# Kernel optimization log

Measured on AMD Instinct MI355X. Metric: run time of the kernel, lower is better.

The kernel has to match this reference:

```python
import jax, jax.numpy as jnp
import numpy as np

N = 100000       # nodes
E0 = 1600000     # random edges (self-loops appended -> E = E0 + N)
IN = 128         # input feature dim
H1, C1 = 8, 8    # conv1 heads, out channels per head
C2 = 64          # num_classes (conv2 out, heads=1)
NEG_SLOPE = 0.2


def gat_conv(x, src, dst, W, att_src, att_dst, bias, heads, out_ch, concat):
    """PyG-style GATConv (eval mode, no dropout). x: [N, F_in]."""
    n = x.shape[0]
    h = (x @ W).reshape(n, heads, out_ch)              # [N, H, C]
    a_src = jnp.sum(h * att_src, axis=-1)              # [N, H]
    a_dst = jnp.sum(h * att_dst, axis=-1)              # [N, H]
    e = jax.nn.leaky_relu(a_src[src] + a_dst[dst], NEG_SLOPE)  # [E, H]
    # segment softmax over edges grouped by destination node
    e_max = jax.ops.segment_max(e, dst, num_segments=n)
    ex = jnp.exp(e - e_max[dst])
    denom = jax.ops.segment_sum(ex, dst, num_segments=n)
    alpha = ex / denom[dst]                            # [E, H]
    msg = h[src] * alpha[:, :, None]                   # [E, H, C]
    out = jax.ops.segment_sum(msg, dst, num_segments=n)  # [N, H, C]
    out = out.reshape(n, heads * out_ch) if concat else out.mean(axis=1)
    return out + bias


def setup_inputs() -> dict:
    key = jax.random.key(0)
    ks = jax.random.split(key, 12)
    nodes = jnp.arange(N, dtype=jnp.int32)
    feat = jax.random.normal(ks[0], (N, IN), jnp.float32)
    src = jax.random.randint(ks[1], (E0,), 0, N, jnp.int32)
    dst = jax.random.randint(ks[2], (E0,), 0, N, jnp.int32)
    loop = jnp.arange(N, dtype=jnp.int32)
    edge_index = jnp.stack([jnp.concatenate([src, loop]),
                            jnp.concatenate([dst, loop])])  # [2, E]
    mask = jnp.ones((N,), bool)
    label = jax.random.randint(ks[3], (N,), 0, C2, jnp.int32)
    s = 0.1
    W1 = jax.random.normal(ks[4], (IN, H1 * C1), jnp.float32) * s
    att_src1 = jax.random.normal(ks[5], (H1, C1), jnp.float32) * s
    att_dst1 = jax.random.normal(ks[6], (H1, C1), jnp.float32) * s
    b1 = jnp.zeros((H1 * C1,), jnp.float32)
    W2 = jax.random.normal(ks[7], (H1 * C1, C2), jnp.float32) * s
    att_src2 = jax.random.normal(ks[8], (1, C2), jnp.float32) * s
    att_dst2 = jax.random.normal(ks[9], (1, C2), jnp.float32) * s
    b2 = jnp.zeros((C2,), jnp.float32)
    return {"nodes": nodes, "feat": feat, "edge_index": edge_index, "mask": mask,
            "label": label, "W1": W1, "att_src1": att_src1, "att_dst1": att_dst1,
            "b1": b1, "W2": W2, "att_src2": att_src2, "att_dst2": att_dst2, "b2": b2}


def reference(nodes, feat, edge_index, mask, label,
              W1, att_src1, att_dst1, b1, W2, att_src2, att_dst2, b2):
    src, dst = edge_index[0], edge_index[1]
    x = jax.nn.elu(gat_conv(feat, src, dst, W1, att_src1, att_dst1, b1,
                            H1, C1, concat=True))          # [N, 64]
    scores = gat_conv(x, src, dst, W2, att_src2, att_dst2, b2,
                      1, C2, concat=False)                  # [N, C2]
    logp = jax.nn.log_softmax(scores, axis=-1)
    nll = -jnp.take_along_axis(logp, label[:, None].astype(jnp.int32), axis=1)[:, 0]
    m = mask.astype(scores.dtype)
    loss = jnp.sum(nll * m) / jnp.sum(m)                    # masked mean CE
    pred = jnp.argmax(scores, axis=1)
    return loss, pred, label
```

## Files before the change

### kernel.cpp

```cpp
#include <hip/hip_runtime.h>
#include <cstdint>

#define NHEAD 8
#define D1 64
#define IN_F 128
#define NEG 0.2f
#define NBINS 256
#define BINS 1024
#define BSH 7
#define CHUNK 8192

__device__ __forceinline__ void fma4(float4& a, float s, const float4& v)
{
    a.x = fmaf(s, v.x, a.x); a.y = fmaf(s, v.y, a.y);
    a.z = fmaf(s, v.z, a.z); a.w = fmaf(s, v.w, a.w);
}

__global__ __launch_bounds__(256) void k_gemm1_hist(
    const float* __restrict__ feat,
    const float* __restrict__ W1,
    const float* __restrict__ att_s,
    const float* __restrict__ att_d,
    float* __restrict__ h1, float* __restrict__ a_src, float* __restrict__ a_dst,
    const int* __restrict__ dst, int* __restrict__ btot, int* __restrict__ bh,
    int N, int E, int GH)
{
    __shared__ float Wh[32 * 64];
    __shared__ float Fh[64 * 36];
    const int tid = threadIdx.x;

    if ((int)blockIdx.x < GH) {
        int* hist = (int*)Wh;
        for (int b = tid; b < BINS; b += 256) hist[b] = 0;
        __syncthreads();
        const int e0 = blockIdx.x * CHUNK;
        #pragma unroll
        for (int r = 0; r < 8; ++r) {
            int e = e0 + r * 1024 + tid * 4;
            if (e + 3 < E) {
                int4 d4 = *(const int4*)&dst[e];
                atomicAdd(&hist[d4.x >> BSH], 1);
                atomicAdd(&hist[d4.y >> BSH], 1);
                atomicAdd(&hist[d4.z >> BSH], 1);
                atomicAdd(&hist[d4.w >> BSH], 1);
            } else {
                for (int k = e; k < E && k < e + 4; ++k)
                    atomicAdd(&hist[dst[k] >> BSH], 1);
            }
        }
        __syncthreads();
        for (int b = tid; b < BINS; b += 256) {
            int c = hist[b];
            bh[(size_t)blockIdx.x * BINS + b] = c;
            if (c) atomicAdd(&btot[b * 16], c);
        }
        return;
    }

    const int tx = tid & 15, ty = tid >> 4;
    const int base = (blockIdx.x - GH) * 64;
    float4 acc0 = {0,0,0,0}, acc1 = {0,0,0,0}, acc2 = {0,0,0,0}, acc3 = {0,0,0,0};

    for (int p = 0; p < 4; ++p) {
        if (p) __syncthreads();
        for (int i = tid; i < 32 * 64; i += 256)
            Wh[i] = W1[p * 2048 + i];
        for (int i = tid; i < 64 * 32; i += 256) {
            int r = i >> 5, kk = i & 31;
            int n = base + r;
            Fh[r * 36 + kk] = (n < N) ? feat[(size_t)n * IN_F + p * 32 + kk] : 0.f;
        }
        __syncthreads();
        const float* wk = &Wh[4 * tx];
        const float* f0 = &Fh[(4 * ty + 0) * 36];
        const float* f1 = &Fh[(4 * ty + 1) * 36];
        const float* f2 = &Fh[(4 * ty + 2) * 36];
        const float* f3 = &Fh[(4 * ty + 3) * 36];
        #pragma unroll
        for (int kk = 0; kk < 32; kk += 4) {
            float4 fa = *(const float4*)&f0[kk];
            float4 fb = *(const float4*)&f1[kk];
            float4 fc = *(const float4*)&f2[kk];
            float4 fd = *(const float4*)&f3[kk];
            float4 w0 = *(const float4*)&wk[(kk + 0) * 64];
            float4 w1 = *(const float4*)&wk[(kk + 1) * 64];
            float4 w2 = *(const float4*)&wk[(kk + 2) * 64];
            float4 w3 = *(const float4*)&wk[(kk + 3) * 64];
            fma4(acc0, fa.x, w0); fma4(acc0, fa.y, w1); fma4(acc0, fa.z, w2); fma4(acc0, fa.w, w3);
            fma4(acc1, fb.x, w0); fma4(acc1, fb.y, w1); fma4(acc1, fb.z, w2); fma4(acc1, fb.w, w3);
            fma4(acc2, fc.x, w0); fma4(acc2, fc.y, w1); fma4(acc2, fc.z, w2); fma4(acc2, fc.w, w3);
            fma4(acc3, fd.x, w0); fma4(acc3, fd.y, w1); fma4(acc3, fd.z, w2); fma4(acc3, fd.w, w3);
        }
    }
    const float4 as4 = *(const float4*)&att_s[4 * tx];
    const float4 ad4 = *(const float4*)&att_d[4 * tx];
    float4 accs[4] = {acc0, acc1, acc2, acc3};
    #pragma unroll
    for (int i = 0; i < 4; ++i) {
        int n = base + 4 * ty + i;
        if (n < N) {
            *(float4*)&h1[(size_t)n * D1 + 4 * tx] = accs[i];
            float ps = accs[i].x * as4.x + accs[i].y * as4.y + accs[i].z * as4.z + accs[i].w * as4.w;
            float pd = accs[i].x * ad4.x + accs[i].y * ad4.y + accs[i].z * ad4.z + accs[i].w * ad4.w;
            ps += __shfl_xor(ps, 1);
            pd += __shfl_xor(pd, 1);
            if ((tx & 1) == 0) {
                a_src[n * NHEAD + (tx >> 1)] = ps;
                a_dst[n * NHEAD + (tx >> 1)] = pd;
            }
        }
    }
}

__device__ __forceinline__ int block_incl_scan(int v, int tid, int* lds4)
{
    int lane = tid & 63, w = tid >> 6;
    #pragma unroll
    for (int off = 1; off < 64; off <<= 1) {
        int t = __shfl_up(v, off);
        if (lane >= off) v += t;
    }
    if (lane == 63) lds4[w] = v;
    __syncthreads();
    int add = 0;
    #pragma unroll
    for (int i = 0; i < 4; ++i)
        if (i < w) add += lds4[i];
    __syncthreads();
    return v + add;
}

__global__ __launch_bounds__(256) void k_bscan(
    const int* __restrict__ btot, int* __restrict__ bbase, int* __restrict__ gcur,
    double* __restrict__ bins)
{
    __shared__ int lds4[4];
    const int tid = threadIdx.x;
    bins[tid] = 0.0;
    int c0 = btot[(4 * tid + 0) * 16];
    int c1 = btot[(4 * tid + 1) * 16];
    int c2 = btot[(4 * tid + 2) * 16];
    int c3 = btot[(4 * tid + 3) * 16];
    int v = c0 + c1 + c2 + c3;
    int incl = block_incl_scan(v, tid, lds4);
    int b0 = incl - v, b1 = b0 + c0, b2 = b1 + c1, b3 = b2 + c2;
    bbase[4 * tid + 0] = b0; gcur[(4 * tid + 0) * 16] = b0;
    bbase[4 * tid + 1] = b1; gcur[(4 * tid + 1) * 16] = b1;
    bbase[4 * tid + 2] = b2; gcur[(4 * tid + 2) * 16] = b2;
    bbase[4 * tid + 3] = b3; gcur[(4 * tid + 3) * 16] = b3;
}

__global__ __launch_bounds__(256) void k_scatter(
    const int* __restrict__ src, const int* __restrict__ dst,
    const int* __restrict__ bh, int* __restrict__ gcur,
    int* __restrict__ bucketed, int E)
{
    __shared__ int base[BINS], cur[BINS];
    const int tid = threadIdx.x;
    for (int b = tid; b < BINS; b += 256) {
        cur[b] = 0;
        int c = bh[(size_t)blockIdx.x * BINS + b];
        if (c) base[b] = atomicAdd(&gcur[b * 16], c);
    }
    __syncthreads();
    const int e0 = blockIdx.x * CHUNK;
    #pragma unroll
    for (int r = 0; r < 8; ++r) {
        int e = e0 + r * 1024 + tid * 4;
        if (e + 3 < E) {
            int4 d4 = *(const int4*)&dst[e];
            int4 s4 = *(const int4*)&src[e];
            int bx, rx;
            bx = d4.x >> BSH; rx = atomicAdd(&cur[bx], 1); bucketed[base[bx] + rx] = ((d4.x & 127) << 17) | s4.x;
            bx = d4.y >> BSH; rx = atomicAdd(&cur[bx], 1); bucketed[base[bx] + rx] = ((d4.y & 127) << 17) | s4.y;
            bx = d4.z >> BSH; rx = atomicAdd(&cur[bx], 1); bucketed[base[bx] + rx] = ((d4.z & 127) << 17) | s4.z;
            bx = d4.w >> BSH; rx = atomicAdd(&cur[bx], 1); bucketed[base[bx] + rx] = ((d4.w & 127) << 17) | s4.w;
        } else {
            for (int k = e; k < E && k < e + 4; ++k) {
                int d = dst[k];
                int bx = d >> BSH;
                int rx = atomicAdd(&cur[bx], 1);
                bucketed[base[bx] + rx] = ((d & 127) << 17) | src[k];
            }
        }
    }
}

__global__ __launch_bounds__(256) void k_seg(
    const int* __restrict__ btot, const int* __restrict__ bbase,
    const int* __restrict__ bucketed,
    int* __restrict__ deg, int* __restrict__ rowstart, int* __restrict__ srcs, int N)
{
    __shared__ int cnt[128], cur[128], lb[128];
    const int tid = threadIdx.x;
    const int b = blockIdx.x;
    const int gs = bbase[b];
    const int sz = btot[b * 16];
    if (tid < 128) { cnt[tid] = 0; cur[tid] = 0; }
    __syncthreads();
    for (int i = tid; i < sz; i += 256)
        atomicAdd(&cnt[bucketed[gs + i] >> 17], 1);
    __syncthreads();
    if (tid < 128) lb[tid] = cnt[tid];
    __syncthreads();
    #pragma unroll
    for (int off = 1; off < 128; off <<= 1) {
        int t = 0;
        if (tid < 128 && tid >= off) t = lb[tid - off];
        __syncthreads();
        if (tid < 128 && tid >= off) lb[tid] += t;
        __syncthreads();
    }
    if (tid < 128) {
        int ex = lb[tid] - cnt[tid];
        lb[tid] = ex;
        int d = b * 128 + tid;
        if (d < N) { deg[d] = cnt[tid]; rowstart[d] = gs + ex; }
    }
    __syncthreads();
    for (int i = tid; i < sz; i += 256) {
        int v = bucketed[gs + i];
        int d7 = v >> 17;
        int r = atomicAdd(&cur[d7], 1);
        srcs[gs + lb[d7] + r] = v & 0x1FFFF;
    }
}

__global__ __launch_bounds__(256) void k_agg1(
    const int* __restrict__ deg, const int* __restrict__ rowstart,
    const int* __restrict__ srcs,
    const float* __restrict__ a_s, const float* __restrict__ a_d,
    const float* __restrict__ h1, const float* __restrict__ b1,
    float* __restrict__ x, int N)
{
    const int tid = threadIdx.x, w = tid >> 6, j = tid & 63;
    const int c = j & 7, hh = j >> 3;
    const int t = j & 15, q = j >> 4;
    const int n = blockIdx.x * 4 + w;
    if (n >= N) return;
    const int rlen = deg[n];
    const int row = rowstart[n];
    const float ad = a_d[n * NHEAD + hh];
    float4 acc = {0.f, 0.f, 0.f, 0.f};
    float den = 0.f;
    int m = rlen < 8 ? rlen : 8;
    int myS   = (c < m) ? srcs[row + c] : 0;
    float av  = (c < m) ? a_s[myS * NHEAD + hh] : 0.f;
    for (int base = 0; base < rlen; base += 8) {
        int mn = rlen - base - 8; if (mn > 8) mn = 8; if (mn < 0) mn = 0;
        int   myS_n = (c < mn) ? srcs[row + base + 8 + c] : 0;
        float av_n  = (c < mn) ? a_s[myS_n * NHEAD + hh] : 0.f;
        float ex = 0.f;
        if (c < m) {
            float v = av + ad;
            v = v > 0.f ? v : NEG * v;
            ex = expf(v);
        }
        float ds = ex;
        ds += __shfl_xor(ds, 1);
        ds += __shfl_xor(ds, 2);
        ds += __shfl_xor(ds, 4);
        den += ds;
        int   s0 = __shfl(myS, 2 * q);
        int   s1 = __shfl(myS, 2 * q + 1);
        float e0 = __shfl(ex, ((t >> 1) << 3) | (2 * q));
        float e1 = __shfl(ex, ((t >> 1) << 3) | (2 * q + 1));
        float4 l0 = *(const float4*)&h1[(size_t)s0 * D1 + 4 * t];
        float4 l1 = *(const float4*)&h1[(size_t)s1 * D1 + 4 * t];
        fma4(acc, e0, l0);
        fma4(acc, e1, l1);
        myS = myS_n; av = av_n; m = mn;
    }
    acc.x += __shfl_xor(acc.x, 16); acc.y += __shfl_xor(acc.y, 16);
    acc.z += __shfl_xor(acc.z, 16); acc.w += __shfl_xor(acc.w, 16);
    acc.x += __shfl_xor(acc.x, 32); acc.y += __shfl_xor(acc.y, 32);
    acc.z += __shfl_xor(acc.z, 32); acc.w += __shfl_xor(acc.w, 32);
    float dd = __shfl(den, (t >> 1) << 3);
    if (q == 0) {
        float4 b = *(const float4*)&b1[4 * t];
        float4 o;
        o.x = acc.x / dd + b.x; o.y = acc.y / dd + b.y;
        o.z = acc.z / dd + b.z; o.w = acc.w / dd + b.w;
        o.x = o.x > 0.f ? o.x : expm1f(o.x);
        o.y = o.y > 0.f ? o.y : expm1f(o.y);
        o.z = o.z > 0.f ? o.z : expm1f(o.z);
        o.w = o.w > 0.f ? o.w : expm1f(o.w);
        *(float4*)&x[(size_t)n * D1 + 4 * t] = o;
    }
}

__global__ __launch_bounds__(256) void k_gemm2(
    const float* __restrict__ x,
    const float* __restrict__ W2,
    const float* __restrict__ att_s,
    const float* __restrict__ att_d,
    float* __restrict__ h2, float* __restrict__ a_src, float* __restrict__ a_dst,
    int N)
{
    __shared__ float Wh[64 * 64];
    __shared__ float Fh[64 * 68];
    const int tid = threadIdx.x;
    const int tx = tid & 15, ty = tid >> 4;
    const int base = blockIdx.x * 64;
    for (int i = tid; i < 64 * 64; i += 256)
        Wh[i] = W2[i];
    for (int i = tid; i < 64 * 64; i += 256) {
        int r = i >> 6, kk = i & 63;
        int n = base + r;
        Fh[r * 68 + kk] = (n < N) ? x[(size_t)n * 64 + kk] : 0.f;
    }
    __syncthreads();
    float4 acc0 = {0,0,0,0}, acc1 = {0,0,0,0}, acc2 = {0,0,0,0}, acc3 = {0,0,0,0};
    const float* wk = &Wh[4 * tx];
    const float* f0 = &Fh[(4 * ty + 0) * 68];
    const float* f1 = &Fh[(4 * ty + 1) * 68];
    const float* f2 = &Fh[(4 * ty + 2) * 68];
    const float* f3 = &Fh[(4 * ty + 3) * 68];
    #pragma unroll 4
    for (int kk = 0; kk < 64; kk += 4) {
        float4 fa = *(const float4*)&f0[kk];
        float4 fb = *(const float4*)&f1[kk];
        float4 fc = *(const float4*)&f2[kk];
        float4 fd = *(const float4*)&f3[kk];
        float4 w0 = *(const float4*)&wk[(kk + 0) * 64];
        float4 w1 = *(const float4*)&wk[(kk + 1) * 64];
        float4 w2 = *(const float4*)&wk[(kk + 2) * 64];
        float4 w3 = *(const float4*)&wk[(kk + 3) * 64];
        fma4(acc0, fa.x, w0); fma4(acc0, fa.y, w1); fma4(acc0, fa.z, w2); fma4(acc0, fa.w, w3);
        fma4(acc1, fb.x, w0); fma4(acc1, fb.y, w1); fma4(acc1, fb.z, w2); fma4(acc1, fb.w, w3);
        fma4(acc2, fc.x, w0); fma4(acc2, fc.y, w1); fma4(acc2, fc.z, w2); fma4(acc2, fc.w, w3);
        fma4(acc3, fd.x, w0); fma4(acc3, fd.y, w1); fma4(acc3, fd.z, w2); fma4(acc3, fd.w, w3);
    }
    const float4 as4 = *(const float4*)&att_s[4 * tx];
    const float4 ad4 = *(const float4*)&att_d[4 * tx];
    float4 accs[4] = {acc0, acc1, acc2, acc3};
    #pragma unroll
    for (int i = 0; i < 4; ++i) {
        int n = base + 4 * ty + i;
        if (n < N) {
            *(float4*)&h2[(size_t)n * 64 + 4 * tx] = accs[i];
            float ps = accs[i].x * as4.x + accs[i].y * as4.y + accs[i].z * as4.z + accs[i].w * as4.w;
            float pd = accs[i].x * ad4.x + accs[i].y * ad4.y + accs[i].z * ad4.z + accs[i].w * ad4.w;
            ps += __shfl_xor(ps, 1); pd += __shfl_xor(pd, 1);
            ps += __shfl_xor(ps, 2); pd += __shfl_xor(pd, 2);
            ps += __shfl_xor(ps, 4); pd += __shfl_xor(pd, 4);
            ps += __shfl_xor(ps, 8); pd += __shfl_xor(pd, 8);
            if (tx == 0) { a_src[n] = ps; a_dst[n] = pd; }
        }
    }
}

__global__ __launch_bounds__(256) void k_agg2(
    const int* __restrict__ deg, const int* __restrict__ rowstart,
    const int* __restrict__ srcs,
    const float* __restrict__ a_s, const float* __restrict__ a_d,
    const float* __restrict__ h2, const float* __restrict__ b2,
    const int* __restrict__ label,
    float* __restrict__ dout, double* __restrict__ bins, int N)
{
    __shared__ int2 sx[4][64];
    __shared__ float snll[16];
    const int tid = threadIdx.x, w = tid >> 6, j = tid & 63;
    const int t = j & 15, g16 = j & 0x30;
    const int n = blockIdx.x * 16 + (tid >> 4);
    if (tid < 16) snll[tid] = 0.f;
    __syncthreads();
    const bool valid = (n < N);
    const int rlen = valid ? deg[n] : 0;
    const int row  = valid ? rowstart[n] : 0;
    const float ad = valid ? a_d[n] : 0.f;
    float4 acc = {0.f, 0.f, 0.f, 0.f};
    float den = 0.f;
    for (int base = 0; base < rlen; base += 16) {
        int m = rlen - base; if (m > 16) m = 16;
        int myS = 0; float ex = 0.f;
        if (t < m) {
            myS = srcs[row + base + t];
            float v = a_s[myS] + ad;
            v = v > 0.f ? v : NEG * v;
            ex = expf(v);
        }
        float ds = ex;
        ds += __shfl_xor(ds, 1); ds += __shfl_xor(ds, 2);
        ds += __shfl_xor(ds, 4); ds += __shfl_xor(ds, 8);
        den += ds;
        sx[w][j] = make_int2(myS, __float_as_int(ex));
        asm volatile("s_waitcnt lgkmcnt(0)" ::: "memory");
        for (int kb = 0; kb < m; kb += 4) {
            int2 p0 = sx[w][g16 | (kb + 0)];
            int2 p1 = sx[w][g16 | (kb + 1)];
            int2 p2 = sx[w][g16 | (kb + 2)];
            int2 p3 = sx[w][g16 | (kb + 3)];
            float4 l0 = *(const float4*)&h2[(size_t)p0.x * 64 + 4 * t];
            float4 l1 = *(const float4*)&h2[(size_t)p1.x * 64 + 4 * t];
            float4 l2 = *(const float4*)&h2[(size_t)p2.x * 64 + 4 * t];
            float4 l3 = *(const float4*)&h2[(size_t)p3.x * 64 + 4 * t];
            fma4(acc, __int_as_float(p0.y), l0);
            fma4(acc, __int_as_float(p1.y), l1);
            fma4(acc, __int_as_float(p2.y), l2);
            fma4(acc, __int_as_float(p3.y), l3);
        }
        asm volatile("s_waitcnt lgkmcnt(0)" ::: "memory");
    }
    float4 b = *(const float4*)&b2[4 * t];
    float4 sc;
    sc.x = acc.x / den + b.x; sc.y = acc.y / den + b.y;
    sc.z = acc.z / den + b.z; sc.w = acc.w / den + b.w;
    float mv = sc.x; int mi = 4 * t;
    if (sc.y > mv) { mv = sc.y; mi = 4 * t + 1; }
    if (sc.z > mv) { mv = sc.z; mi = 4 * t + 2; }
    if (sc.w > mv) { mv = sc.w; mi = 4 * t + 3; }
    #pragma unroll
    for (int off = 1; off < 16; off <<= 1) {
        float ov = __shfl_xor(mv, off);
        int oi = __shfl_xor(mi, off);
        if (ov > mv || (ov == mv && oi < mi)) { mv = ov; mi = oi; }
    }
    float se = expf(sc.x - mv) + expf(sc.y - mv) + expf(sc.z - mv) + expf(sc.w - mv);
    #pragma unroll
    for (int off = 1; off < 16; off <<= 1) se += __shfl_xor(se, off);
    int lab = valid ? label[n] : 0;
    int comp = lab & 3;
    float cl = comp == 0 ? sc.x : comp == 1 ? sc.y : comp == 2 ? sc.z : sc.w;
    float sl = __shfl(cl, g16 | (lab >> 2));
    if (t == 0 && valid) {
        snll[tid >> 4] = mv + logf(se) - sl;
        dout[1 + n] = (float)mi;
        dout[1 + (size_t)N + n] = (float)lab;
    }
    __syncthreads();
    if (tid == 0) {
        double bs = 0.0;
        #pragma unroll
        for (int i = 0; i < 16; ++i) bs += (double)snll[i];
        atomicAdd(&bins[blockIdx.x & (NBINS - 1)], bs);
    }
}

__global__ __launch_bounds__(256) void k_loss(
    const double* __restrict__ bins, float* __restrict__ dout, int N)
{
    __shared__ double sw[4];
    const int tid = threadIdx.x;
    double v = bins[tid];
    #pragma unroll
    for (int off = 1; off < 64; off <<= 1) v += __shfl_xor(v, off);
    if ((tid & 63) == 0) sw[tid >> 6] = v;
    __syncthreads();
    if (tid == 0)
        dout[0] = (float)((sw[0] + sw[1] + sw[2] + sw[3]) / (double)N);
}

extern "C" void kernel_launch(void* const* d_in, const int* in_sizes, int n_in,
                              void* d_out, int out_size, void* d_ws, size_t ws_size,
                              hipStream_t stream)
{
    const float* feat   = (const float*)d_in[1];
    const int*   edge   = (const int*)d_in[2];
    const int*   label  = (const int*)d_in[4];
    const float* W1     = (const float*)d_in[5];
    const float* att_s1 = (const float*)d_in[6];
    const float* att_d1 = (const float*)d_in[7];
    const float* b1     = (const float*)d_in[8];
    const float* W2     = (const float*)d_in[9];
    const float* att_s2 = (const float*)d_in[10];
    const float* att_d2 = (const float*)d_in[11];
    const float* b2     = (const float*)d_in[12];

    const int N = in_sizes[0];
    const int E = in_sizes[2] / 2;
    const int* src = edge;
    const int* dst = edge + E;

    float* bufA = (float*)d_ws;
    float* bufB = bufA + (size_t)N * 64;
    float* a_s1 = bufB + (size_t)N * 64;
    float* a_d1 = a_s1 + (size_t)N * 8;
    int*   deg  = (int*)(a_d1 + (size_t)N * 8);
    int*   rowstart = deg + N;
    int*   srcs = rowstart + N;
    double* bins = (double*)(((uintptr_t)(srcs + E) + 7) & ~(uintptr_t)7);

    int* bucketed = (int*)bufB;
    int* btot  = bucketed + E;
    int* gcur  = btot + BINS * 16;
    int* bbase = gcur + BINS * 16;
    int* bh    = bbase + BINS;

    float* a_s2 = a_s1;
    float* a_d2 = a_s1 + N;

    float* out = (float*)d_out;

    const int GH    = (E + CHUNK - 1) / CHUNK;
    const int G1    = (N + 63) / 64;
    const int NBUCK = (N + 127) / 128;

    hipMemsetAsync(btot, 0, (size_t)BINS * 16 * sizeof(int), stream);

    k_gemm1_hist<<<GH + G1, 256, 0, stream>>>(feat, W1, att_s1, att_d1,
                                              bufA, a_s1, a_d1,
                                              dst, btot, bh, N, E, GH);
    k_bscan  <<<1, 256, 0, stream>>>(btot, bbase, gcur, bins);
    k_scatter<<<GH, 256, 0, stream>>>(src, dst, bh, gcur, bucketed, E);
    k_seg    <<<NBUCK, 256, 0, stream>>>(btot, bbase, bucketed, deg, rowstart, srcs, N);

    k_agg1 <<<(N + 3) / 4, 256, 0, stream>>>(deg, rowstart, srcs, a_s1, a_d1,
                                             bufA, b1, bufB, N);
    k_gemm2<<<G1, 256, 0, stream>>>(bufB, W2, att_s2, att_d2, bufA, a_s2, a_d2, N);
    k_agg2 <<<(N + 15) / 16, 256, 0, stream>>>(deg, rowstart, srcs, a_s2, a_d2,
                                               bufA, b2, label, out, bins, N);
    k_loss <<<1, 256, 0, stream>>>(bins, out, N);
}
```

Baseline: 397.8 us.

## Process 16 edges per wave in layer-1 aggregation with LDS-shared attention weights

Restructures the layer-1 aggregation kernel so that each wave handles 16 edges per iteration instead of 8. Each lane computes two heads' exp weights and stages them in shared memory, then each quarter-wave gathers four source rows per iteration. The per-head denominator is now accumulated alongside the features and reduced with shuffles, which removes the cross-lane shuffle reductions per edge batch. Fast __expf also replaces expf in both aggregation kernels, trading some accuracy for cheaper exponentials.

Result: no change. 390.3 us (-1.9%).

```diff
diff --git a/kernel.cpp b/kernel.cpp
--- a/kernel.cpp
+++ b/kernel.cpp
@@ -233,54 +233,60 @@
     const float* __restrict__ h1, const float* __restrict__ b1,
     float* __restrict__ x, int N)
 {
+    __shared__ float sex[4][128];
     const int tid = threadIdx.x, w = tid >> 6, j = tid & 63;
-    const int c = j & 7, hh = j >> 3;
     const int t = j & 15, q = j >> 4;
     const int n = blockIdx.x * 4 + w;
     if (n >= N) return;
     const int rlen = deg[n];
     const int row = rowstart[n];
-    const float ad = a_d[n * NHEAD + hh];
+    const float2 ad2 = *(const float2*)&a_d[n * NHEAD + 2 * q];
+    const int h = t >> 1;
+    float* sw = sex[w];
     float4 acc = {0.f, 0.f, 0.f, 0.f};
     float den = 0.f;
-    int m = rlen < 8 ? rlen : 8;
-    int myS   = (c < m) ? srcs[row + c] : 0;
-    float av  = (c < m) ? a_s[myS * NHEAD + hh] : 0.f;
-    for (int base = 0; base < rlen; base += 8) {
-        int mn = rlen - base - 8; if (mn > 8) mn = 8; if (mn < 0) mn = 0;
-        int   myS_n = (c < mn) ? srcs[row + base + 8 + c] : 0;
-        float av_n  = (c < mn) ? a_s[myS_n * NHEAD + hh] : 0.f;
-        float ex = 0.f;
-        if (c < m) {
-            float v = av + ad;
-            v = v > 0.f ? v : NEG * v;
-            ex = expf(v);
-        }
-        float ds = ex;
-        ds += __shfl_xor(ds, 1);
-        ds += __shfl_xor(ds, 2);
-        ds += __shfl_xor(ds, 4);
-        den += ds;
-        int   s0 = __shfl(myS, 2 * q);
-        int   s1 = __shfl(myS, 2 * q + 1);
-        float e0 = __shfl(ex, ((t >> 1) << 3) | (2 * q));
-        float e1 = __shfl(ex, ((t >> 1) << 3) | (2 * q + 1));
-        float4 l0 = *(const float4*)&h1[(size_t)s0 * D1 + 4 * t];
-        float4 l1 = *(const float4*)&h1[(size_t)s1 * D1 + 4 * t];
-        fma4(acc, e0, l0);
-        fma4(acc, e1, l1);
-        myS = myS_n; av = av_n; m = mn;
+    bool v = (t < rlen);
+    int   s  = v ? srcs[row + t] : 0;
+    float2 a2 = v ? *(const float2*)&a_s[s * NHEAD + 2 * q] : make_float2(0.f, 0.f);
+    for (int base = 0; base < rlen; base += 16) {
+        bool vn = (base + 16 + t < rlen);
+        int   sn  = vn ? srcs[row + base + 16 + t] : 0;
+        float2 an = vn ? *(const float2*)&a_s[sn * NHEAD + 2 * q] : make_float2(0.f, 0.f);
+        float e0 = 0.f, e1 = 0.f;
+        if (v) {
+            float x0 = a2.x + ad2.x; x0 = x0 > 0.f ? x0 : NEG * x0; e0 = __expf(x0);
+            float x1 = a2.y + ad2.y; x1 = x1 > 0.f ? x1 : NEG * x1; e1 = __expf(x1);
+        }
+        *(float2*)&sw[t * 8 + 2 * q] = make_float2(e0, e1);
+        asm volatile("s_waitcnt lgkmcnt(0)" ::: "memory");
+        int mTot = rlen - base;
+        if (4 * q < mTot) {
+            int s0 = __shfl(s, 4 * q + 0), s1 = __shfl(s, 4 * q + 1);
+            int s2 = __shfl(s, 4 * q + 2), s3 = __shfl(s, 4 * q + 3);
+            float w0 = sw[(4 * q + 0) * 8 + h], w1 = sw[(4 * q + 1) * 8 + h];
+            float w2 = sw[(4 * q + 2) * 8 + h], w3 = sw[(4 * q + 3) * 8 + h];
+            float4 l0 = *(const float4*)&h1[(size_t)s0 * D1 + 4 * t];
+            float4 l1 = *(const float4*)&h1[(size_t)s1 * D1 + 4 * t];
+            float4 l2 = *(const float4*)&h1[(size_t)s2 * D1 + 4 * t];
+            float4 l3 = *(const float4*)&h1[(size_t)s3 * D1 + 4 * t];
+            fma4(acc, w0, l0); fma4(acc, w1, l1);
+            fma4(acc, w2, l2); fma4(acc, w3, l3);
+            den += (w0 + w1) + (w2 + w3);
+        }
+        asm volatile("s_waitcnt lgkmcnt(0)" ::: "memory");
+        v = vn; s = sn; a2 = an;
     }
     acc.x += __shfl_xor(acc.x, 16); acc.y += __shfl_xor(acc.y, 16);
     acc.z += __shfl_xor(acc.z, 16); acc.w += __shfl_xor(acc.w, 16);
+    den   += __shfl_xor(den, 16);
     acc.x += __shfl_xor(acc.x, 32); acc.y += __shfl_xor(acc.y, 32);
     acc.z += __shfl_xor(acc.z, 32); acc.w += __shfl_xor(acc.w, 32);
-    float dd = __shfl(den, (t >> 1) << 3);
+    den   += __shfl_xor(den, 32);
     if (q == 0) {
         float4 b = *(const float4*)&b1[4 * t];
         float4 o;
-        o.x = acc.x / dd + b.x; o.y = acc.y / dd + b.y;
-        o.z = acc.z / dd + b.z; o.w = acc.w / dd + b.w;
+        o.x = acc.x / den + b.x; o.y = acc.y / den + b.y;
+        o.z = acc.z / den + b.z; o.w = acc.w / den + b.w;
         o.x = o.x > 0.f ? o.x : expm1f(o.x);
         o.y = o.y > 0.f ? o.y : expm1f(o.y);
         o.z = o.z > 0.f ? o.z : expm1f(o.z);
@@ -378,7 +384,7 @@
             myS = srcs[row + base + t];
             float v = a_s[myS] + ad;
             v = v > 0.f ? v : NEG * v;
-            ex = expf(v);
+            ex = __expf(v);
         }
         float ds = ex;
         ds += __shfl_xor(ds, 1); ds += __shfl_xor(ds, 2);
@@ -416,7 +422,7 @@
         int oi = __shfl_xor(mi, off);
         if (ov > mv || (ov == mv && oi < mi)) { mv = ov; mi = oi; }
     }
-    float se = expf(sc.x - mv) + expf(sc.y - mv) + expf(sc.z - mv) + expf(sc.w - mv);
+    float se = __expf(sc.x - mv) + __expf(sc.y - mv) + __expf(sc.z - mv) + __expf(sc.w - mv);
     #pragma unroll
     for (int off = 1; off < 16; off <<= 1) se += __shfl_xor(se, off);
     int lab = valid ? label[n] : 0;
```
